# Performance work log

Hardware: AMD Instinct MI355X
Metric: run time of the kernel (lower is better)

## Reference

```python
import jax, jax.numpy as jnp
import numpy as np

N, E, G = 50000, 640000, 256
NODE_IN, EDGE_IN, EXT_IN = 32, 16, 8
H, L = 128, 3
BN_EPS = 1e-5


def _linear_init(key, fan_in, fan_out):
    kw, kb = jax.random.split(key)
    s = 1.0 / np.sqrt(fan_in)
    w = jax.random.uniform(kw, (fan_in, fan_out), minval=-s, maxval=s, dtype=jnp.float32)
    b = jax.random.uniform(kb, (fan_out,), minval=-s, maxval=s, dtype=jnp.float32)
    return w, b


def setup_inputs() -> dict:
    key = jax.random.key(0)
    ks = jax.random.split(key, 16)
    x = jax.random.normal(ks[0], (N, NODE_IN), dtype=jnp.float32)
    edge_index = jax.random.randint(ks[1], (2, E), 0, N)
    edge_attr = jax.random.normal(ks[2], (E, EDGE_IN), dtype=jnp.float32)
    batch = jnp.sort(jax.random.randint(ks[3], (N,), 0, G))
    externals = jax.random.normal(ks[4], (G, EXT_IN), dtype=jnp.float32)

    node_w, node_b = _linear_init(ks[5], NODE_IN, H)
    ee_w1, ee_b1 = _linear_init(ks[6], EDGE_IN, H)
    ee_w2, ee_b2 = _linear_init(ks[7], H, H)
    # stacked per-layer GINEConv MLP params: [L, H, H] / [L, H]
    cks = jax.random.split(ks[8], 2 * L)
    cw1, cb1, cw2, cb2 = [], [], [], []
    for l in range(L):
        w1, b1 = _linear_init(cks[2 * l], H, H)
        w2, b2 = _linear_init(cks[2 * l + 1], H, H)
        cw1.append(w1); cb1.append(b1); cw2.append(w2); cb2.append(b2)
    conv_w1 = jnp.stack(cw1); conv_b1 = jnp.stack(cb1)
    conv_w2 = jnp.stack(cw2); conv_b2 = jnp.stack(cb2)
    bn_gamma = jnp.ones((L, H), dtype=jnp.float32)
    bn_beta = jnp.zeros((L, H), dtype=jnp.float32)
    ext_w1, ext_b1 = _linear_init(ks[9], EXT_IN, H)
    ext_w2, ext_b2 = _linear_init(ks[10], H, H)
    reg_w1, reg_b1 = _linear_init(ks[11], 2 * H, H)
    reg_w2, reg_b2 = _linear_init(ks[12], H, 1)

    return dict(x=x, edge_attr=edge_attr, externals=externals,
                node_w=node_w, node_b=node_b,
                ee_w1=ee_w1, ee_b1=ee_b1, ee_w2=ee_w2, ee_b2=ee_b2,
                conv_w1=conv_w1, conv_b1=conv_b1, conv_w2=conv_w2, conv_b2=conv_b2,
                bn_gamma=bn_gamma, bn_beta=bn_beta,
                ext_w1=ext_w1, ext_b1=ext_b1, ext_w2=ext_w2, ext_b2=ext_b2,
                reg_w1=reg_w1, reg_b1=reg_b1, reg_w2=reg_w2, reg_b2=reg_b2,
                edge_index=edge_index, batch=batch, num_graphs=G)


def reference(x, edge_attr, externals,
              node_w, node_b, ee_w1, ee_b1, ee_w2, ee_b2,
              conv_w1, conv_b1, conv_w2, conv_b2, bn_gamma, bn_beta,
              ext_w1, ext_b1, ext_w2, ext_b2,
              reg_w1, reg_b1, reg_w2, reg_b2,
              edge_index, batch, num_graphs):
    n = x.shape[0]
    src, dst = edge_index[0], edge_index[1]
    h = x @ node_w + node_b                                      # [N,H]
    e = jax.nn.relu(edge_attr @ ee_w1 + ee_b1) @ ee_w2 + ee_b2   # [E,H]
    for l in range(conv_w1.shape[0]):
        # GINEConv (eps=0): aggr = sum_j relu(x_j + e_ij); out = MLP(x_i + aggr)
        msg = jax.nn.relu(h[src] + e)                            # gather + add + relu [E,H]
        aggr = jax.ops.segment_sum(msg, dst, num_segments=n)     # scatter-add [N,H]
        z = h + aggr
        z = jax.nn.relu(z @ conv_w1[l] + conv_b1[l]) @ conv_w2[l] + conv_b2[l]
        # BatchNorm1d (batch statistics)
        mean = z.mean(axis=0)
        var = z.var(axis=0)
        z = (z - mean) * jax.lax.rsqrt(var + BN_EPS) * bn_gamma[l] + bn_beta[l]
        h = jax.nn.relu(z)                                       # dropout = identity (eval)
    # global mean pool over graphs
    gsum = jax.ops.segment_sum(h, batch, num_segments=num_graphs)
    cnt = jax.ops.segment_sum(jnp.ones((n, 1), h.dtype), batch, num_segments=num_graphs)
    graph_emb = gsum / jnp.maximum(cnt, 1.0)
    ext = jax.nn.relu(externals @ ext_w1 + ext_b1) @ ext_w2 + ext_b2
    comb = jnp.concatenate([graph_emb, ext], axis=-1)            # [G,2H]
    out = jax.nn.relu(comb @ reg_w1 + reg_b1) @ reg_w2 + reg_b2  # [G,1]
    return out.squeeze(-1)
```

## Files before the change

kernel.cpp:

```cpp
#include <hip/hip_runtime.h>

typedef __bf16 bf16_t;
typedef __bf16 bf16x8 __attribute__((ext_vector_type(8)));
typedef __bf16 bf16x4 __attribute__((ext_vector_type(4)));
typedef __bf16 bf16x2 __attribute__((ext_vector_type(2)));
typedef float  f32x4  __attribute__((ext_vector_type(4)));

#define MFMA16(a, b, c) __builtin_amdgcn_mfma_f32_16x16x32_bf16((a), (b), (c), 0, 0, 0)

__global__ __launch_bounds__(256) void prep_all_kernel(
    const float* __restrict__ nw,  const float* __restrict__ ew1,
    const float* __restrict__ ew2, const float* __restrict__ cw1,
    const float* __restrict__ cw2,
    bf16_t* __restrict__ nwt,  bf16_t* __restrict__ ew1t,
    bf16_t* __restrict__ ew2t, bf16_t* __restrict__ cw1t,
    bf16_t* __restrict__ cw2t)
{
    int b = blockIdx.x;
    const float* W; bf16_t* O; int Kact, KP, lb;
    if (b < 16)       { W = nw;  O = nwt;  Kact = 32;  KP = 32;  lb = b; }
    else if (b < 32)  { W = ew1; O = ew1t; Kact = 16;  KP = 32;  lb = b - 16; }
    else if (b < 96)  { W = ew2; O = ew2t; Kact = 128; KP = 128; lb = b - 32; }
    else if (b < 288) { int l = (b - 96) / 64;  W = cw1 + l * 16384; O = cw1t + l * 16384;
                        Kact = 128; KP = 128; lb = (b - 96) % 64; }
    else              { int l = (b - 288) / 64; W = cw2 + l * 16384; O = cw2t + l * 16384;
                        Kact = 128; KP = 128; lb = (b - 288) % 64; }
    int idx = lb * 256 + threadIdx.x;
    if (idx >= 128 * KP) return;
    int j    = idx & 7;
    int lane = (idx >> 3) & 63;
    int ct   = (idx >> 9) & 7;
    int kc   = idx >> 12;
    int n = ct * 16 + (lane & 15);
    int k = kc * 32 + (lane >> 4) * 8 + j;
    O[idx] = (bf16_t)((k < Kact) ? W[k * 128 + n] : 0.0f);
}

__global__ __launch_bounds__(256) void hist_kernel(const int* __restrict__ ei,
                                                   int* __restrict__ deg, int E,
                                                   const float* __restrict__ ea) {
    int t = blockIdx.x * 256 + threadIdx.x;
    if (t < E) {
        atomicAdd(&deg[ei[(long)E + t]], 1);
        float w0 = ea[(long)t * 16];
        float w1 = ea[(long)t * 16 + 8];
        asm volatile("" :: "v"(w0), "v"(w1));
    }
}

__global__ __launch_bounds__(256) void scanA_kernel(const int* __restrict__ deg,
                                                    int* __restrict__ partials,
                                                    int* __restrict__ bsums, int N) {
    __shared__ int s[256];
    int b = blockIdx.x, t = threadIdx.x;
    int base = b * 1024 + t * 4;
    int v0 = (base + 0 < N) ? deg[base + 0] : 0;
    int v1 = (base + 1 < N) ? deg[base + 1] : 0;
    int v2 = (base + 2 < N) ? deg[base + 2] : 0;
    int v3 = (base + 3 < N) ? deg[base + 3] : 0;
    int local = v0 + v1 + v2 + v3;
    s[t] = local;
    __syncthreads();
    for (int off = 1; off < 256; off <<= 1) {
        int v = (t >= off) ? s[t - off] : 0;
        __syncthreads();
        s[t] += v;
        __syncthreads();
    }
    int excl = s[t] - local;
    if (base + 0 < N) partials[base + 0] = excl;
    if (base + 1 < N) partials[base + 1] = excl + v0;
    if (base + 2 < N) partials[base + 2] = excl + v0 + v1;
    if (base + 3 < N) partials[base + 3] = excl + v0 + v1 + v2;
    if (t == 255) bsums[b] = s[255];
}

__global__ __launch_bounds__(256) void scanB_kernel(const int* __restrict__ bsums,
                                                    int* __restrict__ boff,
                                                    int* __restrict__ rowptr,
                                                    int NB, int N) {
    __shared__ int s[256];
    int t = threadIdx.x;
    int local = (t < NB) ? bsums[t] : 0;
    s[t] = local;
    __syncthreads();
    for (int off = 1; off < 256; off <<= 1) {
        int v = (t >= off) ? s[t - off] : 0;
        __syncthreads();
        s[t] += v;
        __syncthreads();
    }
    if (t < NB) boff[t] = s[t] - local;
    if (t == NB - 1) rowptr[N] = s[t];
}

__global__ __launch_bounds__(256) void scanC_kernel(const int* __restrict__ partials,
                                                    const int* __restrict__ boff,
                                                    int* __restrict__ rowptr,
                                                    int* __restrict__ cursor, int N) {
    int i = blockIdx.x * 256 + threadIdx.x;
    if (i >= N) return;
    int v = partials[i] + boff[i >> 10];
    rowptr[i] = v;
    cursor[i] = v;
}

__global__ __launch_bounds__(256) void scatter_kernel(const int* __restrict__ ei,
                                                      int* __restrict__ cursor,
                                                      int* __restrict__ srcp,
                                                      int* __restrict__ eorig, int E) {
    int t = blockIdx.x * 256 + threadIdx.x;
    if (t >= E) return;
    int d = ei[(long)E + t];
    int pos = atomicAdd(&cursor[d], 1);
    srcp[pos] = ei[t];
    eorig[pos] = t;
}

__global__ __launch_bounds__(256) void node_enc_kernel(
    const float* __restrict__ A, int M,
    const bf16_t* __restrict__ Ws, const float* __restrict__ bias,
    bf16_t* __restrict__ outp)
{
    constexpr int S = 136;
    __shared__ bf16_t T[128 * S];

    const int  tid  = threadIdx.x;
    const int  wv   = tid >> 6, lane = tid & 63;
    const long row0 = (long)blockIdx.x * 128;
    const int  l16  = lane & 15, quad = lane >> 4;

    {
        int r  = wv * 32 + (lane >> 1);
        long gr = row0 + r;
        int c0 = (lane & 1) * 16;
#pragma unroll
        for (int q = 0; q < 4; ++q) {
            float4 v = make_float4(0.f, 0.f, 0.f, 0.f);
            if (gr < M) v = *(const float4*)(A + gr * 32 + c0 + q * 4);
            bf16_t* d = &T[r * S + c0 + q * 4];
            d[0] = (bf16_t)v.x; d[1] = (bf16_t)v.y; d[2] = (bf16_t)v.z; d[3] = (bf16_t)v.w;
        }
    }

    f32x4 acc[2][8];
#pragma unroll
    for (int r = 0; r < 2; r++)
#pragma unroll
        for (int c = 0; c < 8; c++) acc[r][c] = (f32x4){0.f, 0.f, 0.f, 0.f};

    {
        bf16x8 af0 = *(const bf16x8*)&T[(wv * 32 + l16) * S + quad * 8];
        bf16x8 af1 = *(const bf16x8*)&T[(wv * 32 + 16 + l16) * S + quad * 8];
#pragma unroll
        for (int c = 0; c < 8; c++) {
            bf16x8 bfr = *(const bf16x8*)&Ws[((c * 64) + lane) * 8];
            acc[0][c] = MFMA16(af0, bfr, acc[0][c]);
            acc[1][c] = MFMA16(af1, bfr, acc[1][c]);
        }
    }

#pragma unroll
    for (int r = 0; r < 2; r++) {
        int mrow = wv * 32 + r * 16 + quad * 4;
#pragma unroll
        for (int c = 0; c < 8; c++) {
            int col = c * 16 + l16;
            float bb = bias[col];
#pragma unroll
            for (int q = 0; q < 4; q++)
                T[(mrow + q) * S + col] = (bf16_t)(acc[r][c][q] + bb);
        }
    }

#pragma unroll
    for (int it = 0; it < 8; ++it) {
        int idx = it * 64 + lane;
        int row = wv * 32 + (idx >> 4);
        int seg = idx & 15;
        long grow = row0 + row;
        if (grow < M)
            *(uint4*)&outp[grow * 128 + seg * 8] = *(const uint4*)&T[row * S + seg * 8];
    }
}

__global__ __launch_bounds__(256) void edge_mlp_kernel(
    const float* __restrict__ A, int M,
    const bf16_t* __restrict__ Ws1, const float* __restrict__ b1,
    const bf16_t* __restrict__ Ws2, const float* __restrict__ b2,
    const int* __restrict__ eorig, bf16_t* __restrict__ outp)
{
    constexpr int S = 136;
    __shared__ bf16_t T[64 * S];

    const int  tid  = threadIdx.x;
    const int  wv   = tid >> 6, lane = tid & 63;
    const long row0 = (long)blockIdx.x * 64;
    const int  l16  = lane & 15, quad = lane >> 4;

    {
        int  r  = wv * 16 + (lane >> 2);
        long gr = row0 + r;
        float4 v = make_float4(0.f, 0.f, 0.f, 0.f);
        if (gr < M) {
            long eo = eorig[gr];
            v = *(const float4*)(A + eo * 16 + (lane & 3) * 4);
        }
        bf16_t* d = &T[r * S + (lane & 3) * 4];
        d[0] = (bf16_t)v.x; d[1] = (bf16_t)v.y; d[2] = (bf16_t)v.z; d[3] = (bf16_t)v.w;
    }

    f32x4 acc[8];
#pragma unroll
    for (int c = 0; c < 8; c++) acc[c] = (f32x4){0.f, 0.f, 0.f, 0.f};

    {
        bf16x8 af;
#pragma unroll
        for (int j = 0; j < 8; ++j) af[j] = (bf16_t)0.f;
        if (quad < 2) af = *(const bf16x8*)&T[(wv * 16 + l16) * S + quad * 8];
#pragma unroll
        for (int c = 0; c < 8; c++) {
            bf16x8 bfr = *(const bf16x8*)&Ws1[((c * 64) + lane) * 8];
            acc[c] = MFMA16(af, bfr, acc[c]);
        }
    }

    const int mbase = wv * 16 + quad * 4;

#pragma unroll
    for (int c = 0; c < 8; c++) {
        int col = c * 16 + l16;
        float bb = b1[col];
#pragma unroll
        for (int q = 0; q < 4; q++)
            T[(mbase + q) * S + col] = (bf16_t)fmaxf(acc[c][q] + bb, 0.f);
    }

#pragma unroll
    for (int c = 0; c < 8; c++) acc[c] = (f32x4){0.f, 0.f, 0.f, 0.f};

#pragma unroll
    for (int kc = 0; kc < 4; ++kc) {
        bf16x8 af = *(const bf16x8*)&T[(wv * 16 + l16) * S + kc * 32 + quad * 8];
#pragma unroll
        for (int c = 0; c < 8; c++) {
            bf16x8 bfr = *(const bf16x8*)&Ws2[(((kc * 8 + c) * 64) + lane) * 8];
            acc[c] = MFMA16(af, bfr, acc[c]);
        }
    }

#pragma unroll
    for (int c = 0; c < 8; c++) {
        int col = c * 16 + l16;
        float bb = b2[col];
#pragma unroll
        for (int q = 0; q < 4; q++)
            T[(mbase + q) * S + col] = (bf16_t)(acc[c][q] + bb);
    }

#pragma unroll
    for (int it = 0; it < 4; ++it) {
        int idx = it * 64 + lane;
        int row = wv * 16 + (idx >> 4);
        int seg = idx & 15;
        long grow = row0 + row;
        if (grow < M)
            *(uint4*)&outp[grow * 128 + seg * 8] = *(const uint4*)&T[row * S + seg * 8];
    }
}

__global__ __launch_bounds__(256) void bnx_kernel(
    const bf16_t* __restrict__ z, const float* __restrict__ bns,
    const float* __restrict__ gamma, const float* __restrict__ beta,
    bf16_t* __restrict__ hbuf, int N)
{
    long t = (long)blockIdx.x * 256 + threadIdx.x;
    long i0 = t * 8;
    if (i0 >= (long)N * 128) return;
    int c = (int)(i0 & 127);
    const float invN = 1.f / (float)N;
    bf16x8 v = *(const bf16x8*)(z + i0);
    bf16x8 o;
#pragma unroll
    for (int u = 0; u < 8; ++u) {
        int cc = c + u;
        float m  = bns[cc] * invN;
        float va = bns[128 + cc] * invN - m * m;
        float iv = rsqrtf(va + 1e-5f);
        float sc = gamma[cc] * iv;
        float sh = beta[cc] - m * sc;
        o[u] = (bf16_t)fmaxf((float)v[u] * sc + sh, 0.f);
    }
    *(bf16x8*)(hbuf + i0) = o;
}

__global__ __launch_bounds__(512, 8) void aggr_conv_kernel(
    const bf16_t* __restrict__ xin,
    const bf16_t* __restrict__ e,
    const int* __restrict__ rowptr, const int* __restrict__ srcp, int M,
    const bf16_t* __restrict__ Ws1, const float* __restrict__ b1,
    const bf16_t* __restrict__ Ws2, const float* __restrict__ b2,
    bf16_t* __restrict__ zout, float* __restrict__ bn_out)
{
    constexpr int S = 136;
    __shared__ bf16_t T[32 * S];
    __shared__ float  wred[2][256];

    const int  tid  = threadIdx.x;
    const int  wv   = tid >> 6, lane = tid & 63;
    const long row0 = (long)blockIdx.x * 32;
    const int  l16  = lane & 15, quad = lane >> 4;

    const long nbase = row0 + wv * 4;
    int rpv = 0;
    {
        long idx = nbase + lane;
        if (idx > M) idx = M;
        if (lane <= 4) rpv = rowptr[idx];
    }

#pragma unroll 1
    for (int ri = 0; ri < 4; ++ri) {
        const int  r   = wv * 4 + ri;
        const long n   = row0 + r;
        const int  beg = __shfl(rpv, ri);
        const int  end = __shfl(rpv, ri + 1);
        float ax = 0.f, ay = 0.f;
        if (n < M) {
            bf16x2 xv = *(const bf16x2*)(xin + n * 128 + lane * 2);
            ax = (float)xv[0]; ay = (float)xv[1];
            for (int base = beg; base < end; base += 64) {
                int cnt = min(64, end - base);
                int sv  = (base + lane < end) ? srcp[base + lane] : 0;
                int j = 0;
                for (; j + 3 < cnt; j += 4) {
                    int s0 = __shfl(sv, j),     s1 = __shfl(sv, j + 1);
                    int s2 = __shfl(sv, j + 2), s3 = __shfl(sv, j + 3);
                    bf16x2 x0 = *(const bf16x2*)(xin + (long)s0 * 128 + lane * 2);
                    bf16x2 x1 = *(const bf16x2*)(xin + (long)s1 * 128 + lane * 2);
                    bf16x2 x2 = *(const bf16x2*)(xin + (long)s2 * 128 + lane * 2);
                    bf16x2 x3 = *(const bf16x2*)(xin + (long)s3 * 128 + lane * 2);
                    bf16x2 e0 = *(const bf16x2*)(e + (long)(base + j + 0) * 128 + lane * 2);
                    bf16x2 e1 = *(const bf16x2*)(e + (long)(base + j + 1) * 128 + lane * 2);
                    bf16x2 e2 = *(const bf16x2*)(e + (long)(base + j + 2) * 128 + lane * 2);
                    bf16x2 e3 = *(const bf16x2*)(e + (long)(base + j + 3) * 128 + lane * 2);
                    ax += fmaxf((float)x0[0] + (float)e0[0], 0.f);
                    ay += fmaxf((float)x0[1] + (float)e0[1], 0.f);
                    ax += fmaxf((float)x1[0] + (float)e1[0], 0.f);
                    ay += fmaxf((float)x1[1] + (float)e1[1], 0.f);
                    ax += fmaxf((float)x2[0] + (float)e2[0], 0.f);
                    ay += fmaxf((float)x2[1] + (float)e2[1], 0.f);
                    ax += fmaxf((float)x3[0] + (float)e3[0], 0.f);
                    ay += fmaxf((float)x3[1] + (float)e3[1], 0.f);
                }
                for (; j < cnt; ++j) {
                    int s0 = __shfl(sv, j);
                    bf16x2 x0 = *(const bf16x2*)(xin + (long)s0 * 128 + lane * 2);
                    bf16x2 e0 = *(const bf16x2*)(e + (long)(base + j) * 128 + lane * 2);
                    ax += fmaxf((float)x0[0] + (float)e0[0], 0.f);
                    ay += fmaxf((float)x0[1] + (float)e0[1], 0.f);
                }
            }
        }
        bf16x2 o; o[0] = (bf16_t)ax; o[1] = (bf16_t)ay;
        *(bf16x2*)&T[r * S + lane * 2] = o;
    }
    __syncthreads();

    const int rb = wv >> 2, cq = wv & 3;
    const int mbase = rb * 16 + quad * 4;

    f32x4 acc[2];
#pragma unroll
    for (int c = 0; c < 2; c++) acc[c] = (f32x4){0.f, 0.f, 0.f, 0.f};

#pragma unroll
    for (int kc = 0; kc < 4; ++kc) {
        bf16x8 af = *(const bf16x8*)&T[(rb * 16 + l16) * S + kc * 32 + quad * 8];
#pragma unroll
        for (int c = 0; c < 2; c++) {
            int ct = cq * 2 + c;
            bf16x8 bfr = *(const bf16x8*)&Ws1[(((kc * 8 + ct) * 64) + lane) * 8];
            acc[c] = MFMA16(af, bfr, acc[c]);
        }
    }
    __syncthreads();

#pragma unroll
    for (int c = 0; c < 2; c++) {
        int col = (cq * 2 + c) * 16 + l16;
        float bb = b1[col];
#pragma unroll
        for (int q = 0; q < 4; q++)
            T[(mbase + q) * S + col] = (bf16_t)fmaxf(acc[c][q] + bb, 0.f);
    }
    __syncthreads();

#pragma unroll
    for (int c = 0; c < 2; c++) acc[c] = (f32x4){0.f, 0.f, 0.f, 0.f};

#pragma unroll
    for (int kc = 0; kc < 4; ++kc) {
        bf16x8 af = *(const bf16x8*)&T[(rb * 16 + l16) * S + kc * 32 + quad * 8];
#pragma unroll
        for (int c = 0; c < 2; c++) {
            int ct = cq * 2 + c;
            bf16x8 bfr = *(const bf16x8*)&Ws2[(((kc * 8 + ct) * 64) + lane) * 8];
            acc[c] = MFMA16(af, bfr, acc[c]);
        }
    }
    __syncthreads();

#pragma unroll
    for (int c = 0; c < 2; c++) {
        int col = (cq * 2 + c) * 16 + l16;
        float bb = b2[col];
        float s = 0.f, s2 = 0.f;
#pragma unroll
        for (int q = 0; q < 4; q++) {
            float v = acc[c][q] + bb;
            T[(mbase + q) * S + col] = (bf16_t)v;
            if (row0 + mbase + q < M) { s += v; s2 += v * v; }
        }
        s  += __shfl_xor(s, 16);  s  += __shfl_xor(s, 32);
        s2 += __shfl_xor(s2, 16); s2 += __shfl_xor(s2, 32);
        if (quad == 0) {
            wred[rb][col]       = s;
            wred[rb][128 + col] = s2;
        }
    }
    __syncthreads();

    {
        int row = tid >> 4, seg = tid & 15;
        long grow = row0 + row;
        if (grow < M)
            *(uint4*)&zout[grow * 128 + seg * 8] = *(const uint4*)&T[row * S + seg * 8];
    }
    if (tid < 256) {
        float v = wred[0][tid] + wred[1][tid];
        atomicAdd(&bn_out[tid], v);
    }
}

__global__ __launch_bounds__(128) void pool_kernel(
    const bf16_t* __restrict__ z, const float* __restrict__ bns,
    const float* __restrict__ gamma, const float* __restrict__ beta,
    const int* __restrict__ batch,
    float* __restrict__ gsum, float* __restrict__ cnt, int N)
{
    int c = threadIdx.x;
    float mean = bns[c] / (float)N;
    float var  = bns[128 + c] / (float)N - mean * mean;
    float inv  = rsqrtf(var + 1e-5f);
    float sc   = gamma[c] * inv;
    float sh   = beta[c] - mean * sc;
    int n0 = blockIdx.x * 32;
    int n1 = min(n0 + 32, N);
    float acc = 0.f;
    int cur = -1, rc = 0;
    for (int n = n0; n < n1; ++n) {
        int g = batch[n];
        if (g != cur) {
            if (cur >= 0) {
                atomicAdd(&gsum[(long)cur * 128 + c], acc);
                if (c == 0) atomicAdd(&cnt[cur], (float)rc);
            }
            cur = g; acc = 0.f; rc = 0;
        }
        acc += fmaxf((float)z[(long)n * 128 + c] * sc + sh, 0.f);
        rc++;
    }
    if (cur >= 0) {
        atomicAdd(&gsum[(long)cur * 128 + c], acc);
        if (c == 0) atomicAdd(&cnt[cur], (float)rc);
    }
}

__global__ __launch_bounds__(128) void head_kernel(
    const float* __restrict__ gsum, const float* __restrict__ cnt,
    const float* __restrict__ ext_in,
    const float* __restrict__ ew1, const float* __restrict__ eb1,
    const float* __restrict__ ew2, const float* __restrict__ eb2,
    const float* __restrict__ rw1, const float* __restrict__ rb1,
    const float* __restrict__ rw2, const float* __restrict__ rb2,
    float* __restrict__ out)
{
    int g = blockIdx.x, c = threadIdx.x;
    __shared__ float sx[8];
    __shared__ float h1[128];
    __shared__ float comb[256];
    __shared__ float red[128];

    if (c < 8) sx[c] = ext_in[g * 8 + c];
    __syncthreads();
    float a = eb1[c];
#pragma unroll
    for (int k = 0; k < 8; k++) a += sx[k] * ew1[k * 128 + c];
    h1[c] = fmaxf(a, 0.f);
    __syncthreads();
    float b = eb2[c];
    for (int k = 0; k < 128; k++) b += h1[k] * ew2[k * 128 + c];
    comb[c]       = gsum[(long)g * 128 + c] / fmaxf(cnt[g], 1.0f);
    comb[128 + c] = b;
    __syncthreads();
    float r = rb1[c];
    for (int k = 0; k < 256; k++) r += comb[k] * rw1[k * 128 + c];
    r = fmaxf(r, 0.f);
    red[c] = r * rw2[c];
    __syncthreads();
    if (c == 0) {
        float s = rb2[0];
        for (int k = 0; k < 128; k++) s += red[k];
        out[g] = s;
    }
}

extern "C" void kernel_launch(void* const* d_in, const int* in_sizes, int n_in,
                              void* d_out, int out_size, void* d_ws, size_t ws_size,
                              hipStream_t stream)
{
    const float* x         = (const float*)d_in[0];
    const float* edge_attr = (const float*)d_in[1];
    const float* externals = (const float*)d_in[2];
    const float* node_w    = (const float*)d_in[3];
    const float* node_b    = (const float*)d_in[4];
    const float* ee_w1     = (const float*)d_in[5];
    const float* ee_b1     = (const float*)d_in[6];
    const float* ee_w2     = (const float*)d_in[7];
    const float* ee_b2     = (const float*)d_in[8];
    const float* conv_w1   = (const float*)d_in[9];
    const float* conv_b1   = (const float*)d_in[10];
    const float* conv_w2   = (const float*)d_in[11];
    const float* conv_b2   = (const float*)d_in[12];
    const float* bn_gamma  = (const float*)d_in[13];
    const float* bn_beta   = (const float*)d_in[14];
    const float* ext_w1    = (const float*)d_in[15];
    const float* ext_b1    = (const float*)d_in[16];
    const float* ext_w2    = (const float*)d_in[17];
    const float* ext_b2    = (const float*)d_in[18];
    const float* reg_w1    = (const float*)d_in[19];
    const float* reg_b1    = (const float*)d_in[20];
    const float* reg_w2    = (const float*)d_in[21];
    const float* reg_b2    = (const float*)d_in[22];
    const int* edge_index  = (const int*)d_in[23];
    const int* batch       = (const int*)d_in[24];

    const int N = in_sizes[0] / 32;
    const int E = in_sizes[1] / 16;
    const int G = in_sizes[2] / 8;
    const int NB = (N + 1023) / 1024;

    char* p = (char*)d_ws;
    auto alloc = [&](size_t bytes) -> void* {
        void* r = (void*)p;
        p += (bytes + 255) & ~(size_t)255;
        return r;
    };
    bf16_t* h       = (bf16_t*)alloc((size_t)N * 128 * 2);
    bf16_t* zA      = (bf16_t*)alloc((size_t)N * 128 * 2);
    bf16_t* zB      = (bf16_t*)alloc((size_t)N * 128 * 2);
    bf16_t* hb      = (bf16_t*)alloc((size_t)N * 128 * 2);
    bf16_t* ebuf    = (bf16_t*)alloc((size_t)E * 128 * 2);
    int*    deg     = (int*)alloc((size_t)N * 4);
    int*    rowptr  = (int*)alloc(((size_t)N + 1) * 4);
    int*    cursor  = (int*)alloc((size_t)N * 4);
    int*    partials= (int*)alloc((size_t)N * 4);
    int*    bsums   = (int*)alloc((size_t)NB * 4);
    int*    boff    = (int*)alloc((size_t)NB * 4);
    int*    srcp    = (int*)alloc((size_t)E * 4);
    int*    eorig   = (int*)alloc((size_t)E * 4);
    bf16_t* node_wt = (bf16_t*)alloc(128 * 32 * 2);
    bf16_t* ee_w1t  = (bf16_t*)alloc(128 * 32 * 2);
    bf16_t* ee_w2t  = (bf16_t*)alloc(128 * 128 * 2);
    bf16_t* cw1t    = (bf16_t*)alloc(3 * 128 * 128 * 2);
    bf16_t* cw2t    = (bf16_t*)alloc(3 * 128 * 128 * 2);
    float*  bns     = (float*)alloc(3 * 256 * 4);
    float*  gsum    = (float*)alloc((size_t)G * 128 * 4);
    float*  cnt     = (float*)alloc((size_t)G * 4);

    hipMemsetAsync(deg, 0, (size_t)N * 4, stream);
    hipMemsetAsync(bns, 0, 3 * 256 * 4, stream);
    hist_kernel<<<(E + 255) / 256, 256, 0, stream>>>(edge_index, deg, E, edge_attr);
    scanA_kernel<<<NB, 256, 0, stream>>>(deg, partials, bsums, N);
    scanB_kernel<<<1, 256, 0, stream>>>(bsums, boff, rowptr, NB, N);
    scanC_kernel<<<(N + 255) / 256, 256, 0, stream>>>(partials, boff, rowptr, cursor, N);
    scatter_kernel<<<(E + 255) / 256, 256, 0, stream>>>(edge_index, cursor, srcp, eorig, E);

    prep_all_kernel<<<480, 256, 0, stream>>>(node_w, ee_w1, ee_w2, conv_w1, conv_w2,
                                             node_wt, ee_w1t, ee_w2t, cw1t, cw2t);

    node_enc_kernel<<<(N + 127) / 128, 256, 0, stream>>>(x, N, node_wt, node_b, h);

    edge_mlp_kernel<<<(E + 63) / 64, 256, 0, stream>>>(
        edge_attr, E, ee_w1t, ee_b1, ee_w2t, ee_b2, eorig, ebuf);

    const int nblk = (N + 31) / 32;
    const int bblk = ((N * 128 / 8) + 255) / 256;
    aggr_conv_kernel<<<nblk, 512, 0, stream>>>(
        h, ebuf, rowptr, srcp, N,
        cw1t + 0 * 16384, conv_b1 + 0 * 128, cw2t + 0 * 16384, conv_b2 + 0 * 128,
        zA, bns + 0);
    bnx_kernel<<<bblk, 256, 0, stream>>>(zA, bns + 0, bn_gamma + 0, bn_beta + 0, hb, N);
    aggr_conv_kernel<<<nblk, 512, 0, stream>>>(
        hb, ebuf, rowptr, srcp, N,
        cw1t + 1 * 16384, conv_b1 + 1 * 128, cw2t + 1 * 16384, conv_b2 + 1 * 128,
        zB, bns + 256);
    bnx_kernel<<<bblk, 256, 0, stream>>>(zB, bns + 256, bn_gamma + 128, bn_beta + 128, hb, N);
    aggr_conv_kernel<<<nblk, 512, 0, stream>>>(
        hb, ebuf, rowptr, srcp, N,
        cw1t + 2 * 16384, conv_b1 + 2 * 128, cw2t + 2 * 16384, conv_b2 + 2 * 128,
        zA, bns + 512);

    hipMemsetAsync(gsum, 0, (size_t)G * 128 * 4, stream);
    hipMemsetAsync(cnt, 0, (size_t)G * 4, stream);
    pool_kernel<<<(N + 31) / 32, 128, 0, stream>>>(zA, bns + 512, bn_gamma + 256, bn_beta + 256,
                                                   batch, gsum, cnt, N);
    head_kernel<<<G, 128, 0, stream>>>(gsum, cnt, externals,
                                       ext_w1, ext_b1, ext_w2, ext_b2,
                                       reg_w1, reg_b1, reg_w2, reg_b2,
                                       (float*)d_out);
}
```

Before: 563.3 us.

## Use persistent work-stealing blocks over 16-row tiles in aggregation-conv kernel

The fused aggregation+MLP kernel becomes a persistent kernel. A fixed grid of 256-thread blocks pulls 16-node tiles from a global atomic cursor, replacing one 512-thread block per 32 nodes. This targets load imbalance from variable node degree and the tail effect, and the edge-gather inner loop is unrolled to 8 to keep more loads in flight. In exchange it adds an atomic plus extra barriers per tile, more BN-stat atomics (one set per 16 rows instead of per 32), and a small memset of the cursors.

New measurement: 747.8 us. +32.7%, slower.

```diff
diff --git a/kernel.cpp b/kernel.cpp
--- a/kernel.cpp
+++ b/kernel.cpp
@@ -295,152 +295,195 @@
     *(bf16x8*)(hbuf + i0) = o;
 }
 
-__global__ __launch_bounds__(512, 8) void aggr_conv_kernel(
+__global__ __launch_bounds__(256, 8) void aggr_conv_kernel(
     const bf16_t* __restrict__ xin,
     const bf16_t* __restrict__ e,
     const int* __restrict__ rowptr, const int* __restrict__ srcp, int M,
+    int ntiles, int* __restrict__ tile_cursor,
     const bf16_t* __restrict__ Ws1, const float* __restrict__ b1,
     const bf16_t* __restrict__ Ws2, const float* __restrict__ b2,
     bf16_t* __restrict__ zout, float* __restrict__ bn_out)
 {
     constexpr int S = 136;
-    __shared__ bf16_t T[32 * S];
-    __shared__ float  wred[2][256];
-
-    const int  tid  = threadIdx.x;
-    const int  wv   = tid >> 6, lane = tid & 63;
-    const long row0 = (long)blockIdx.x * 32;
-    const int  l16  = lane & 15, quad = lane >> 4;
-
-    const long nbase = row0 + wv * 4;
-    int rpv = 0;
-    {
-        long idx = nbase + lane;
-        if (idx > M) idx = M;
-        if (lane <= 4) rpv = rowptr[idx];
-    }
+    __shared__ bf16_t T[16 * S];
+    __shared__ float  wred[256];
+    __shared__ int    tileslot;
+
+    const int tid  = threadIdx.x;
+    const int wv   = tid >> 6, lane = tid & 63;
+    const int l16  = lane & 15, quad = lane >> 4;
+
+    for (;;) {
+        if (tid == 0) tileslot = atomicAdd(tile_cursor, 1);
+        __syncthreads();
+        const int tile = tileslot;
+        if (tile >= ntiles) return;
+        const long row0 = (long)tile * 16;
+
+        int rpv = 0;
+        {
+            long idx = row0 + wv * 4 + lane;
+            if (idx > M) idx = M;
+            if (lane <= 4) rpv = rowptr[idx];
+        }
 
 #pragma unroll 1
-    for (int ri = 0; ri < 4; ++ri) {
-        const int  r   = wv * 4 + ri;
-        const long n   = row0 + r;
-        const int  beg = __shfl(rpv, ri);
-        const int  end = __shfl(rpv, ri + 1);
-        float ax = 0.f, ay = 0.f;
-        if (n < M) {
-            bf16x2 xv = *(const bf16x2*)(xin + n * 128 + lane * 2);
-            ax = (float)xv[0]; ay = (float)xv[1];
-            for (int base = beg; base < end; base += 64) {
-                int cnt = min(64, end - base);
-                int sv  = (base + lane < end) ? srcp[base + lane] : 0;
-                int j = 0;
-                for (; j + 3 < cnt; j += 4) {
-                    int s0 = __shfl(sv, j),     s1 = __shfl(sv, j + 1);
-                    int s2 = __shfl(sv, j + 2), s3 = __shfl(sv, j + 3);
-                    bf16x2 x0 = *(const bf16x2*)(xin + (long)s0 * 128 + lane * 2);
-                    bf16x2 x1 = *(const bf16x2*)(xin + (long)s1 * 128 + lane * 2);
-                    bf16x2 x2 = *(const bf16x2*)(xin + (long)s2 * 128 + lane * 2);
-                    bf16x2 x3 = *(const bf16x2*)(xin + (long)s3 * 128 + lane * 2);
-                    bf16x2 e0 = *(const bf16x2*)(e + (long)(base + j + 0) * 128 + lane * 2);
-                    bf16x2 e1 = *(const bf16x2*)(e + (long)(base + j + 1) * 128 + lane * 2);
-                    bf16x2 e2 = *(const bf16x2*)(e + (long)(base + j + 2) * 128 + lane * 2);
-                    bf16x2 e3 = *(const bf16x2*)(e + (long)(base + j + 3) * 128 + lane * 2);
-                    ax += fmaxf((float)x0[0] + (float)e0[0], 0.f);
-                    ay += fmaxf((float)x0[1] + (float)e0[1], 0.f);
-                    ax += fmaxf((float)x1[0] + (float)e1[0], 0.f);
-                    ay += fmaxf((float)x1[1] + (float)e1[1], 0.f);
-                    ax += fmaxf((float)x2[0] + (float)e2[0], 0.f);
-                    ay += fmaxf((float)x2[1] + (float)e2[1], 0.f);
-                    ax += fmaxf((float)x3[0] + (float)e3[0], 0.f);
-                    ay += fmaxf((float)x3[1] + (float)e3[1], 0.f);
-                }
-                for (; j < cnt; ++j) {
-                    int s0 = __shfl(sv, j);
-                    bf16x2 x0 = *(const bf16x2*)(xin + (long)s0 * 128 + lane * 2);
-                    bf16x2 e0 = *(const bf16x2*)(e + (long)(base + j) * 128 + lane * 2);
-                    ax += fmaxf((float)x0[0] + (float)e0[0], 0.f);
-                    ay += fmaxf((float)x0[1] + (float)e0[1], 0.f);
+        for (int ri = 0; ri < 4; ++ri) {
+            const int  r   = wv * 4 + ri;
+            const long n   = row0 + r;
+            const int  beg = __shfl(rpv, ri);
+            const int  end = __shfl(rpv, ri + 1);
+            float ax = 0.f, ay = 0.f;
+            if (n < M) {
+                bf16x2 xv = *(const bf16x2*)(xin + n * 128 + lane * 2);
+                ax = (float)xv[0]; ay = (float)xv[1];
+                for (int base = beg; base < end; base += 64) {
+                    int cnt = min(64, end - base);
+                    int sv  = (base + lane < end) ? srcp[base + lane] : 0;
+                    int j = 0;
+                    for (; j + 7 < cnt; j += 8) {
+                        int s0 = __shfl(sv, j),     s1 = __shfl(sv, j + 1);
+                        int s2 = __shfl(sv, j + 2), s3 = __shfl(sv, j + 3);
+                        int s4 = __shfl(sv, j + 4), s5 = __shfl(sv, j + 5);
+                        int s6 = __shfl(sv, j + 6), s7 = __shfl(sv, j + 7);
+                        bf16x2 x0 = *(const bf16x2*)(xin + (long)s0 * 128 + lane * 2);
+                        bf16x2 x1 = *(const bf16x2*)(xin + (long)s1 * 128 + lane * 2);
+                        bf16x2 x2 = *(const bf16x2*)(xin + (long)s2 * 128 + lane * 2);
+                        bf16x2 x3 = *(const bf16x2*)(xin + (long)s3 * 128 + lane * 2);
+                        bf16x2 x4 = *(const bf16x2*)(xin + (long)s4 * 128 + lane * 2);
+                        bf16x2 x5 = *(const bf16x2*)(xin + (long)s5 * 128 + lane * 2);
+                        bf16x2 x6 = *(const bf16x2*)(xin + (long)s6 * 128 + lane * 2);
+                        bf16x2 x7 = *(const bf16x2*)(xin + (long)s7 * 128 + lane * 2);
+                        bf16x2 e0 = *(const bf16x2*)(e + (long)(base + j + 0) * 128 + lane * 2);
+                        bf16x2 e1 = *(const bf16x2*)(e + (long)(base + j + 1) * 128 + lane * 2);
+                        bf16x2 e2 = *(const bf16x2*)(e + (long)(base + j + 2) * 128 + lane * 2);
+                        bf16x2 e3 = *(const bf16x2*)(e + (long)(base + j + 3) * 128 + lane * 2);
+                        bf16x2 e4 = *(const bf16x2*)(e + (long)(base + j + 4) * 128 + lane * 2);
+                        bf16x2 e5 = *(const bf16x2*)(e + (long)(base + j + 5) * 128 + lane * 2);
+                        bf16x2 e6 = *(const bf16x2*)(e + (long)(base + j + 6) * 128 + lane * 2);
+                        bf16x2 e7 = *(const bf16x2*)(e + (long)(base + j + 7) * 128 + lane * 2);
+                        ax += fmaxf((float)x0[0] + (float)e0[0], 0.f);
+                        ay += fmaxf((float)x0[1] + (float)e0[1], 0.f);
+                        ax += fmaxf((float)x1[0] + (float)e1[0], 0.f);
+                        ay += fmaxf((float)x1[1] + (float)e1[1], 0.f);
+                        ax += fmaxf((float)x2[0] + (float)e2[0], 0.f);
+                        ay += fmaxf((float)x2[1] + (float)e2[1], 0.f);
+                        ax += fmaxf((float)x3[0] + (float)e3[0], 0.f);
+                        ay += fmaxf((float)x3[1] + (float)e3[1], 0.f);
+                        ax += fmaxf((float)x4[0] + (float)e4[0], 0.f);
+                        ay += fmaxf((float)x4[1] + (float)e4[1], 0.f);
+                        ax += fmaxf((float)x5[0] + (float)e5[0], 0.f);
+                        ay += fmaxf((float)x5[1] + (float)e5[1], 0.f);
+                        ax += fmaxf((float)x6[0] + (float)e6[0], 0.f);
+                        ay += fmaxf((float)x6[1] + (float)e6[1], 0.f);
+                        ax += fmaxf((float)x7[0] + (float)e7[0], 0.f);
+                        ay += fmaxf((float)x7[1] + (float)e7[1], 0.f);
+                    }
+                    for (; j + 3 < cnt; j += 4) {
+                        int s0 = __shfl(sv, j),     s1 = __shfl(sv, j + 1);
+                        int s2 = __shfl(sv, j + 2), s3 = __shfl(sv, j + 3);
+                        bf16x2 x0 = *(const bf16x2*)(xin + (long)s0 * 128 + lane * 2);
+                        bf16x2 x1 = *(const bf16x2*)(xin + (long)s1 * 128 + lane * 2);
+                        bf16x2 x2 = *(const bf16x2*)(xin + (long)s2 * 128 + lane * 2);
+                        bf16x2 x3 = *(const bf16x2*)(xin + (long)s3 * 128 + lane * 2);
+                        bf16x2 e0 = *(const bf16x2*)(e + (long)(base + j + 0) * 128 + lane * 2);
+                        bf16x2 e1 = *(const bf16x2*)(e + (long)(base + j + 1) * 128 + lane * 2);
+                        bf16x2 e2 = *(const bf16x2*)(e + (long)(base + j + 2) * 128 + lane * 2);
+                        bf16x2 e3 = *(const bf16x2*)(e + (long)(base + j + 3) * 128 + lane * 2);
+                        ax += fmaxf((float)x0[0] + (float)e0[0], 0.f);
+                        ay += fmaxf((float)x0[1] + (float)e0[1], 0.f);
+                        ax += fmaxf((float)x1[0] + (float)e1[0], 0.f);
+                        ay += fmaxf((float)x1[1] + (float)e1[1], 0.f);
+                        ax += fmaxf((float)x2[0] + (float)e2[0], 0.f);
+                        ay += fmaxf((float)x2[1] + (float)e2[1], 0.f);
+                        ax += fmaxf((float)x3[0] + (float)e3[0], 0.f);
+                        ay += fmaxf((float)x3[1] + (float)e3[1], 0.f);
+                    }
+                    for (; j < cnt; ++j) {
+                        int s0 = __shfl(sv, j);
+                        bf16x2 x0 = *(const bf16x2*)(xin + (long)s0 * 128 + lane * 2);
+                        bf16x2 e0 = *(const bf16x2*)(e + (long)(base + j) * 128 + lane * 2);
+                        ax += fmaxf((float)x0[0] + (float)e0[0], 0.f);
+                        ay += fmaxf((float)x0[1] + (float)e0[1], 0.f);
+                    }
                 }
             }
-        }
-        bf16x2 o; o[0] = (bf16_t)ax; o[1] = (bf16_t)ay;
-        *(bf16x2*)&T[r * S + lane * 2] = o;
-    }
-    __syncthreads();
-
-    const int rb = wv >> 2, cq = wv & 3;
-    const int mbase = rb * 16 + quad * 4;
-
-    f32x4 acc[2];
-#pragma unroll
-    for (int c = 0; c < 2; c++) acc[c] = (f32x4){0.f, 0.f, 0.f, 0.f};
-
-#pragma unroll
-    for (int kc = 0; kc < 4; ++kc) {
-        bf16x8 af = *(const bf16x8*)&T[(rb * 16 + l16) * S + kc * 32 + quad * 8];
+            bf16x2 o; o[0] = (bf16_t)ax; o[1] = (bf16_t)ay;
+            *(bf16x2*)&T[r * S + lane * 2] = o;
+        }
+        __syncthreads();
+
+        const int mbase = quad * 4;
+
+        f32x4 acc[2];
+#pragma unroll
+        for (int c = 0; c < 2; c++) acc[c] = (f32x4){0.f, 0.f, 0.f, 0.f};
+
+#pragma unroll
+        for (int kc = 0; kc < 4; ++kc) {
+            bf16x8 af = *(const bf16x8*)&T[l16 * S + kc * 32 + quad * 8];
+#pragma unroll
+            for (int c = 0; c < 2; c++) {
+                int ct = wv * 2 + c;
+                bf16x8 bfr = *(const bf16x8*)&Ws1[(((kc * 8 + ct) * 64) + lane) * 8];
+                acc[c] = MFMA16(af, bfr, acc[c]);
+            }
+        }
+        __syncthreads();
+
 #pragma unroll
         for (int c = 0; c < 2; c++) {
-            int ct = cq * 2 + c;
-            bf16x8 bfr = *(const bf16x8*)&Ws1[(((kc * 8 + ct) * 64) + lane) * 8];
-            acc[c] = MFMA16(af, bfr, acc[c]);
-        }
-    }
-    __syncthreads();
-
-#pragma unroll
-    for (int c = 0; c < 2; c++) {
-        int col = (cq * 2 + c) * 16 + l16;
-        float bb = b1[col];
-#pragma unroll
-        for (int q = 0; q < 4; q++)
-            T[(mbase + q) * S + col] = (bf16_t)fmaxf(acc[c][q] + bb, 0.f);
-    }
-    __syncthreads();
-
-#pragma unroll
-    for (int c = 0; c < 2; c++) acc[c] = (f32x4){0.f, 0.f, 0.f, 0.f};
-
-#pragma unroll
-    for (int kc = 0; kc < 4; ++kc) {
-        bf16x8 af = *(const bf16x8*)&T[(rb * 16 + l16) * S + kc * 32 + quad * 8];
+            int col = (wv * 2 + c) * 16 + l16;
+            float bb = b1[col];
+#pragma unroll
+            for (int q = 0; q < 4; q++)
+                T[(mbase + q) * S + col] = (bf16_t)fmaxf(acc[c][q] + bb, 0.f);
+        }
+        __syncthreads();
+
+#pragma unroll
+        for (int c = 0; c < 2; c++) acc[c] = (f32x4){0.f, 0.f, 0.f, 0.f};
+
+#pragma unroll
+        for (int kc = 0; kc < 4; ++kc) {
+            bf16x8 af = *(const bf16x8*)&T[l16 * S + kc * 32 + quad * 8];
+#pragma unroll
+            for (int c = 0; c < 2; c++) {
+                int ct = wv * 2 + c;
+                bf16x8 bfr = *(const bf16x8*)&Ws2[(((kc * 8 + ct) * 64) + lane) * 8];
+                acc[c] = MFMA16(af, bfr, acc[c]);
+            }
+        }
+        __syncthreads();
+
 #pragma unroll
         for (int c = 0; c < 2; c++) {
-            int ct = cq * 2 + c;
-            bf16x8 bfr = *(const bf16x8*)&Ws2[(((kc * 8 + ct) * 64) + lane) * 8];
-            acc[c] = MFMA16(af, bfr, acc[c]);
-        }
-    }
-    __syncthreads();
-
-#pragma unroll
-    for (int c = 0; c < 2; c++) {
-        int col = (cq * 2 + c) * 16 + l16;
-        float bb = b2[col];
-        float s = 0.f, s2 = 0.f;
-#pragma unroll
-        for (int q = 0; q < 4; q++) {
-            float v = acc[c][q] + bb;
-            T[(mbase + q) * S + col] = (bf16_t)v;
-            if (row0 + mbase + q < M) { s += v; s2 += v * v; }
-        }
-        s  += __shfl_xor(s, 16);  s  += __shfl_xor(s, 32);
-        s2 += __shfl_xor(s2, 16); s2 += __shfl_xor(s2, 32);
-        if (quad == 0) {
-            wred[rb][col]       = s;
-            wred[rb][128 + col] = s2;
-        }
-    }
-    __syncthreads();
-
-    {
-        int row = tid >> 4, seg = tid & 15;
-        long grow = row0 + row;
-        if (grow < M)
-            *(uint4*)&zout[grow * 128 + seg * 8] = *(const uint4*)&T[row * S + seg * 8];
-    }
-    if (tid < 256) {
-        float v = wred[0][tid] + wred[1][tid];
-        atomicAdd(&bn_out[tid], v);
+            int col = (wv * 2 + c) * 16 + l16;
+            float bb = b2[col];
+            float s = 0.f, s2 = 0.f;
+#pragma unroll
+            for (int q = 0; q < 4; q++) {
+                float v = acc[c][q] + bb;
+                T[(mbase + q) * S + col] = (bf16_t)v;
+                if (row0 + mbase + q < M) { s += v; s2 += v * v; }
+            }
+            s  += __shfl_xor(s, 16);  s  += __shfl_xor(s, 32);
+            s2 += __shfl_xor(s2, 16); s2 += __shfl_xor(s2, 32);
+            if (quad == 0) {
+                wred[col]       = s;
+                wred[128 + col] = s2;
+            }
+        }
+        __syncthreads();
+
+        {
+            int row = tid >> 4, seg = tid & 15;
+            long grow = row0 + row;
+            if (grow < M)
+                *(uint4*)&zout[grow * 128 + seg * 8] = *(const uint4*)&T[row * S + seg * 8];
+        }
+        atomicAdd(&bn_out[tid], wred[tid]);
+        __syncthreads();
     }
 }
 
@@ -577,11 +620,13 @@
     bf16_t* cw1t    = (bf16_t*)alloc(3 * 128 * 128 * 2);
     bf16_t* cw2t    = (bf16_t*)alloc(3 * 128 * 128 * 2);
     float*  bns     = (float*)alloc(3 * 256 * 4);
+    int*    tcur    = (int*)alloc(3 * 4);
     float*  gsum    = (float*)alloc((size_t)G * 128 * 4);
     float*  cnt     = (float*)alloc((size_t)G * 4);
 
     hipMemsetAsync(deg, 0, (size_t)N * 4, stream);
     hipMemsetAsync(bns, 0, 3 * 256 * 4, stream);
+    hipMemsetAsync(tcur, 0, 3 * 4, stream);
     hist_kernel<<<(E + 255) / 256, 256, 0, stream>>>(edge_index, deg, E, edge_attr);
     scanA_kernel<<<NB, 256, 0, stream>>>(deg, partials, bsums, N);
     scanB_kernel<<<1, 256, 0, stream>>>(bsums, boff, rowptr, NB, N);
@@ -596,20 +641,21 @@
     edge_mlp_kernel<<<(E + 63) / 64, 256, 0, stream>>>(
         edge_attr, E, ee_w1t, ee_b1, ee_w2t, ee_b2, eorig, ebuf);
 
-    const int nblk = (N + 31) / 32;
+    const int ntiles = (N + 15) / 16;
+    const int pblk   = min(ntiles, 2048);
     const int bblk = ((N * 128 / 8) + 255) / 256;
-    aggr_conv_kernel<<<nblk, 512, 0, stream>>>(
-        h, ebuf, rowptr, srcp, N,
+    aggr_conv_kernel<<<pblk, 256, 0, stream>>>(
+        h, ebuf, rowptr, srcp, N, ntiles, tcur + 0,
         cw1t + 0 * 16384, conv_b1 + 0 * 128, cw2t + 0 * 16384, conv_b2 + 0 * 128,
         zA, bns + 0);
     bnx_kernel<<<bblk, 256, 0, stream>>>(zA, bns + 0, bn_gamma + 0, bn_beta + 0, hb, N);
-    aggr_conv_kernel<<<nblk, 512, 0, stream>>>(
-        hb, ebuf, rowptr, srcp, N,
+    aggr_conv_kernel<<<pblk, 256, 0, stream>>>(
+        hb, ebuf, rowptr, srcp, N, ntiles, tcur + 1,
         cw1t + 1 * 16384, conv_b1 + 1 * 128, cw2t + 1 * 16384, conv_b2 + 1 * 128,
         zB, bns + 256);
     bnx_kernel<<<bblk, 256, 0, stream>>>(zB, bns + 256, bn_gamma + 128, bn_beta + 128, hb, N);
-    aggr_conv_kernel<<<nblk, 512, 0, stream>>>(
-        hb, ebuf, rowptr, srcp, N,
+    aggr_conv_kernel<<<pblk, 256, 0, stream>>>(
+        hb, ebuf, rowptr, srcp, N, ntiles, tcur + 2,
         cw1t + 2 * 16384, conv_b1 + 2 * 128, cw2t + 2 * 16384, conv_b2 + 2 * 128,
         zA, bns + 512);
 
```
